# Kernel tuning notes

Measured on AMD Instinct MI355X. Metric: run time of the kernel, lower is better.

## Reference

```python
import jax, jax.numpy as jnp
import numpy as np

S, B, N, H = 64, 32, 325, 64

def setup_inputs() -> dict:
    key = jax.random.key(0)
    k1, k2, k3, k4 = jax.random.split(key, 4)
    return {
        "encoder_outputs": jax.random.normal(k1, (S, B, N, H), dtype=jnp.float32),
        "decoder_hidden": jax.random.normal(k2, (B, N, H), dtype=jnp.float32),
        "W": jax.random.normal(k3, (H, H), dtype=jnp.float32) * (1.0 / np.sqrt(H)),
        "b": jax.random.normal(k4, (H,), dtype=jnp.float32) * 0.01,
    }

def reference(encoder_outputs, decoder_hidden, W, b):
    # energy: (S,B,N,H) -- Linear + tanh
    energy = jnp.tanh(jnp.einsum('sbnh,kh->sbnk', encoder_outputs, W) + b)
    # broadcast multiply by decoder_hidden (B,N,H) and reduce over hidden dim -> (S,B,N)
    e = jnp.einsum('sbnh,bnh->sbn', energy, decoder_hidden)
    # softmax over seq_len, output (B,N,S)
    return jax.nn.softmax(jnp.transpose(e, (1, 2, 0)), axis=-1)
```

## Files before the change

### kernel.cpp

```cpp
#include <hip/hip_runtime.h>


constexpr int S = 64, B = 32, N = 325, H = 64;
constexpr int BN = B * N;
constexpr int SBN = S * BN;

typedef __attribute__((ext_vector_type(8))) short short8;
typedef __attribute__((ext_vector_type(4))) float f32x4;

union FragU { unsigned u[4]; short8 s8; uint4 v4; };

__device__ inline unsigned pack_hi(float x0, float x1, float& r0, float& r1) {
    unsigned u0 = __builtin_bit_cast(unsigned, x0);
    unsigned u1 = __builtin_bit_cast(unsigned, x1);
    r0 = x0 - __builtin_bit_cast(float, u0 & 0xffff0000u);
    r1 = x1 - __builtin_bit_cast(float, u1 & 0xffff0000u);
    return (u0 >> 16) | (u1 & 0xffff0000u);
}
__device__ inline unsigned pack_bf(float x0, float x1) {
    return (__builtin_bit_cast(unsigned, x0) >> 16) |
           (__builtin_bit_cast(unsigned, x1) & 0xffff0000u);
}

__global__ void pack_w(const float* __restrict__ W, uint4* __restrict__ wp) {
    int idx = blockIdx.x * blockDim.x + threadIdx.x;
    if (idx >= 512) return;
    int q = idx >> 7, kc = (idx >> 6) & 1, lane = idx & 63;
    int col = lane & 15, grp = lane >> 4;
    const float4* wpt = (const float4*)(W + (q * 16 + col) * H + kc * 32 + grp * 8);
    float4 w0 = wpt[0], w1 = wpt[1];
    float r0, r1, r2, r3, r4, r5, r6, r7;
    FragU hi, lo;
    hi.u[0] = pack_hi(w0.x, w0.y, r0, r1);
    hi.u[1] = pack_hi(w0.z, w0.w, r2, r3);
    hi.u[2] = pack_hi(w1.x, w1.y, r4, r5);
    hi.u[3] = pack_hi(w1.z, w1.w, r6, r7);
    lo.u[0] = pack_bf(r0, r1); lo.u[1] = pack_bf(r2, r3);
    lo.u[2] = pack_bf(r4, r5); lo.u[3] = pack_bf(r6, r7);
    wp[((q * 2 + kc) * 2 + 0) * 64 + lane] = hi.v4;
    wp[((q * 2 + kc) * 2 + 1) * 64 + lane] = lo.v4;
}

__global__ __launch_bounds__(256) void energy_k(
    const float* __restrict__ enc, const float* __restrict__ dec,
    const float* __restrict__ bias, const uint4* __restrict__ wp,
    float* __restrict__ e)
{
    const int lane = threadIdx.x & 63;
    const int wv   = threadIdx.x >> 6;
    const int col  = lane & 15, grp = lane >> 4;
    const int row0 = (blockIdx.x * 4 + wv) * 32;

    FragU a_hi[2][2], a_lo[2][2];
#pragma unroll
    for (int mt = 0; mt < 2; ++mt) {
        const float* er = enc + (row0 + mt * 16 + col) * H;
#pragma unroll
        for (int kc = 0; kc < 2; ++kc) {
            const float4* p4 = (const float4*)(er + kc * 32 + grp * 8);
            float4 x0 = p4[0], x1 = p4[1];
            float r0, r1, r2, r3, r4, r5, r6, r7;
            a_hi[mt][kc].u[0] = pack_hi(x0.x, x0.y, r0, r1);
            a_hi[mt][kc].u[1] = pack_hi(x0.z, x0.w, r2, r3);
            a_hi[mt][kc].u[2] = pack_hi(x1.x, x1.y, r4, r5);
            a_hi[mt][kc].u[3] = pack_hi(x1.z, x1.w, r6, r7);
            a_lo[mt][kc].u[0] = pack_bf(r0, r1);
            a_lo[mt][kc].u[1] = pack_bf(r2, r3);
            a_lo[mt][kc].u[2] = pack_bf(r4, r5);
            a_lo[mt][kc].u[3] = pack_bf(r6, r7);
        }
    }

    int doff[2][4];
#pragma unroll
    for (int mt = 0; mt < 2; ++mt)
#pragma unroll
        for (int r = 0; r < 4; ++r) {
            unsigned sbn = (unsigned)(row0 + mt * 16 + grp * 4 + r);
            unsigned bn  = sbn % (unsigned)BN;
            doff[mt][r]  = (int)(bn * H) + col;
        }

    float bias_v[4];
#pragma unroll
    for (int q = 0; q < 4; ++q) bias_v[q] = bias[q * 16 + col];

    float part[2][4];
#pragma unroll
    for (int mt = 0; mt < 2; ++mt)
#pragma unroll
        for (int r = 0; r < 4; ++r) part[mt][r] = 0.0f;

#pragma unroll
    for (int q = 0; q < 4; ++q) {
        f32x4 acc[2];
        acc[0] = (f32x4){0.f, 0.f, 0.f, 0.f};
        acc[1] = (f32x4){0.f, 0.f, 0.f, 0.f};
#pragma unroll
        for (int kc = 0; kc < 2; ++kc) {
            FragU bh, bl;
            bh.v4 = wp[((q * 2 + kc) * 2 + 0) * 64 + lane];
            bl.v4 = wp[((q * 2 + kc) * 2 + 1) * 64 + lane];
#pragma unroll
            for (int mt = 0; mt < 2; ++mt) {
                acc[mt] = __builtin_amdgcn_mfma_f32_16x16x32_bf16(a_hi[mt][kc].s8, bh.s8, acc[mt], 0, 0, 0);
                acc[mt] = __builtin_amdgcn_mfma_f32_16x16x32_bf16(a_lo[mt][kc].s8, bh.s8, acc[mt], 0, 0, 0);
                acc[mt] = __builtin_amdgcn_mfma_f32_16x16x32_bf16(a_hi[mt][kc].s8, bl.s8, acc[mt], 0, 0, 0);
            }
        }
#pragma unroll
        for (int mt = 0; mt < 2; ++mt)
#pragma unroll
            for (int r = 0; r < 4; ++r) {
                float a = acc[mt][r] + bias_v[q];
                float t = 1.0f - 2.0f * __builtin_amdgcn_rcpf(__expf(2.0f * a) + 1.0f);
                part[mt][r] = fmaf(t, dec[doff[mt][r] + q * 16], part[mt][r]);
            }
    }

#pragma unroll
    for (int mt = 0; mt < 2; ++mt)
#pragma unroll
        for (int r = 0; r < 4; ++r) {
            float v = part[mt][r];
            v += __shfl_xor(v, 1, 64);
            v += __shfl_xor(v, 2, 64);
            v += __shfl_xor(v, 4, 64);
            v += __shfl_xor(v, 8, 64);
            part[mt][r] = v;
        }

    float va = (col & 1) ? part[0][1] : part[0][0];
    float vb = (col & 1) ? part[0][3] : part[0][2];
    float vc = (col & 1) ? part[1][1] : part[1][0];
    float vd = (col & 1) ? part[1][3] : part[1][2];
    float ve = (col & 2) ? vb : va;
    float vf = (col & 2) ? vd : vc;
    float vo = (col & 4) ? vf : ve;
    if (col < 8)
        e[row0 + ((col >> 2) & 1) * 16 + grp * 4 + (col & 3)] = vo;
}

__global__ __launch_bounds__(256) void softmax_k(
    const float* __restrict__ e,
    float* __restrict__ out)
{
    __shared__ float Et[64 * 65];
    __shared__ float Mred[4][64], Sred[4][64], Mfin[64], Rfin[64];

    const int t = threadIdx.x;
    const int bn0 = blockIdx.x * 64;
    const int lane = t & 63, w = t >> 6;

#pragma unroll
    for (int i = 0; i < 16; ++i) {
        int s = w * 16 + i;
        float v = (bn0 + lane < BN) ? e[s * BN + bn0 + lane] : 0.0f;
        Et[s * 65 + lane] = v;
    }
    __syncthreads();

    {
        const int bn_loc = t & 63, sq = t >> 6;
        float m = -1e30f;
#pragma unroll
        for (int i = 0; i < 16; ++i)
            m = fmaxf(m, Et[(sq * 16 + i) * 65 + bn_loc]);
        Mred[sq][bn_loc] = m;
    }
    __syncthreads();
    {
        const int bn_loc = t & 63, sq = t >> 6;
        float m = fmaxf(fmaxf(Mred[0][bn_loc], Mred[1][bn_loc]),
                        fmaxf(Mred[2][bn_loc], Mred[3][bn_loc]));
        float sum = 0.0f;
#pragma unroll
        for (int i = 0; i < 16; ++i)
            sum += __expf(Et[(sq * 16 + i) * 65 + bn_loc] - m);
        Sred[sq][bn_loc] = sum;
        if (sq == 0) Mfin[bn_loc] = m;
    }
    __syncthreads();
    if ((t >> 6) == 0) {
        const int bn_loc = t & 63;
        float sum = Sred[0][bn_loc] + Sred[1][bn_loc] + Sred[2][bn_loc] + Sred[3][bn_loc];
        Rfin[bn_loc] = __builtin_amdgcn_rcpf(sum);
    }
    __syncthreads();

    const int s_out = t & 63, bq = t >> 6;
#pragma unroll
    for (int j = 0; j < 16; ++j) {
        int bn_loc = bq * 16 + j;
        if (bn0 + bn_loc < BN) {
            float p = __expf(Et[s_out * 65 + bn_loc] - Mfin[bn_loc]) * Rfin[bn_loc];
            out[(bn0 + bn_loc) * S + s_out] = p;
        }
    }
}

extern "C" void kernel_launch(void* const* d_in, const int* in_sizes, int n_in,
                              void* d_out, int out_size, void* d_ws, size_t ws_size,
                              hipStream_t stream) {
    const float* enc  = (const float*)d_in[0];
    const float* dec  = (const float*)d_in[1];
    const float* W    = (const float*)d_in[2];
    const float* bias = (const float*)d_in[3];
    float* out        = (float*)d_out;

    uint4* wp = (uint4*)d_ws;
    float* e  = (float*)((char*)d_ws + 65536);

    pack_w<<<2, 256, 0, stream>>>(W, wp);
    energy_k<<<SBN / 128, 256, 0, stream>>>(enc, dec, bias, wp, e);
    softmax_k<<<(BN + 63) / 64, 256, 0, stream>>>(e, out);
}
```

Before: 254.0 us.

## Process four row tiles per wave with register prefetch of next encoder tile

```diff
diff --git a/kernel.cpp b/kernel.cpp
--- a/kernel.cpp
+++ b/kernel.cpp
@@ -4,6 +4,8 @@
 constexpr int S = 64, B = 32, N = 325, H = 64;
 constexpr int BN = B * N;
 constexpr int SBN = S * BN;
+constexpr int NWAVE = SBN / 128;
+constexpr int NBLK = NWAVE / 4;
 
 typedef __attribute__((ext_vector_type(8))) short short8;
 typedef __attribute__((ext_vector_type(4))) float f32x4;
@@ -49,96 +51,136 @@
     const int lane = threadIdx.x & 63;
     const int wv   = threadIdx.x >> 6;
     const int col  = lane & 15, grp = lane >> 4;
-    const int row0 = (blockIdx.x * 4 + wv) * 32;
-
-    FragU a_hi[2][2], a_lo[2][2];
-#pragma unroll
-    for (int mt = 0; mt < 2; ++mt) {
-        const float* er = enc + (row0 + mt * 16 + col) * H;
-#pragma unroll
-        for (int kc = 0; kc < 2; ++kc) {
-            const float4* p4 = (const float4*)(er + kc * 32 + grp * 8);
-            float4 x0 = p4[0], x1 = p4[1];
-            float r0, r1, r2, r3, r4, r5, r6, r7;
-            a_hi[mt][kc].u[0] = pack_hi(x0.x, x0.y, r0, r1);
-            a_hi[mt][kc].u[1] = pack_hi(x0.z, x0.w, r2, r3);
-            a_hi[mt][kc].u[2] = pack_hi(x1.x, x1.y, r4, r5);
-            a_hi[mt][kc].u[3] = pack_hi(x1.z, x1.w, r6, r7);
-            a_lo[mt][kc].u[0] = pack_bf(r0, r1);
-            a_lo[mt][kc].u[1] = pack_bf(r2, r3);
-            a_lo[mt][kc].u[2] = pack_bf(r4, r5);
-            a_lo[mt][kc].u[3] = pack_bf(r6, r7);
-        }
-    }
-
-    int doff[2][4];
-#pragma unroll
-    for (int mt = 0; mt < 2; ++mt)
-#pragma unroll
-        for (int r = 0; r < 4; ++r) {
-            unsigned sbn = (unsigned)(row0 + mt * 16 + grp * 4 + r);
-            unsigned bn  = sbn % (unsigned)BN;
-            doff[mt][r]  = (int)(bn * H) + col;
-        }
+    const int wave_id = blockIdx.x * 4 + wv;
+    const int row_base = wave_id * 128;
 
     float bias_v[4];
 #pragma unroll
     for (int q = 0; q < 4; ++q) bias_v[q] = bias[q * 16 + col];
 
-    float part[2][4];
-#pragma unroll
-    for (int mt = 0; mt < 2; ++mt)
-#pragma unroll
-        for (int r = 0; r < 4; ++r) part[mt][r] = 0.0f;
-
-#pragma unroll
-    for (int q = 0; q < 4; ++q) {
-        f32x4 acc[2];
-        acc[0] = (f32x4){0.f, 0.f, 0.f, 0.f};
-        acc[1] = (f32x4){0.f, 0.f, 0.f, 0.f};
-#pragma unroll
-        for (int kc = 0; kc < 2; ++kc) {
-            FragU bh, bl;
-            bh.v4 = wp[((q * 2 + kc) * 2 + 0) * 64 + lane];
-            bl.v4 = wp[((q * 2 + kc) * 2 + 1) * 64 + lane];
+    float4 raw[8];
+
+    {
+#pragma unroll
+        for (int mt = 0; mt < 2; ++mt) {
+            const float4* er = (const float4*)(enc + (size_t)(row_base + mt * 16 + col) * H) + grp * 2;
+#pragma unroll
+            for (int kc = 0; kc < 2; ++kc) {
+                raw[mt * 4 + kc * 2 + 0] = er[kc * 8 + 0];
+                raw[mt * 4 + kc * 2 + 1] = er[kc * 8 + 1];
+            }
+        }
+    }
+
+    unsigned bnv[2][4];
+
+#pragma unroll
+    for (int t = 0; t < 4; ++t) {
+        const int row0 = row_base + t * 32;
+
+        FragU a_hi[2][2], a_lo[2][2];
+#pragma unroll
+        for (int mt = 0; mt < 2; ++mt)
+#pragma unroll
+            for (int kc = 0; kc < 2; ++kc) {
+                float4 x0 = raw[mt * 4 + kc * 2 + 0];
+                float4 x1 = raw[mt * 4 + kc * 2 + 1];
+                float r0, r1, r2, r3, r4, r5, r6, r7;
+                a_hi[mt][kc].u[0] = pack_hi(x0.x, x0.y, r0, r1);
+                a_hi[mt][kc].u[1] = pack_hi(x0.z, x0.w, r2, r3);
+                a_hi[mt][kc].u[2] = pack_hi(x1.x, x1.y, r4, r5);
+                a_hi[mt][kc].u[3] = pack_hi(x1.z, x1.w, r6, r7);
+                a_lo[mt][kc].u[0] = pack_bf(r0, r1);
+                a_lo[mt][kc].u[1] = pack_bf(r2, r3);
+                a_lo[mt][kc].u[2] = pack_bf(r4, r5);
+                a_lo[mt][kc].u[3] = pack_bf(r6, r7);
+            }
+
+        if (t < 3) {
+            const int rown = row_base + (t + 1) * 32;
 #pragma unroll
             for (int mt = 0; mt < 2; ++mt) {
-                acc[mt] = __builtin_amdgcn_mfma_f32_16x16x32_bf16(a_hi[mt][kc].s8, bh.s8, acc[mt], 0, 0, 0);
-                acc[mt] = __builtin_amdgcn_mfma_f32_16x16x32_bf16(a_lo[mt][kc].s8, bh.s8, acc[mt], 0, 0, 0);
-                acc[mt] = __builtin_amdgcn_mfma_f32_16x16x32_bf16(a_hi[mt][kc].s8, bl.s8, acc[mt], 0, 0, 0);
-            }
-        }
+                const float4* er = (const float4*)(enc + (size_t)(rown + mt * 16 + col) * H) + grp * 2;
+#pragma unroll
+                for (int kc = 0; kc < 2; ++kc) {
+                    raw[mt * 4 + kc * 2 + 0] = er[kc * 8 + 0];
+                    raw[mt * 4 + kc * 2 + 1] = er[kc * 8 + 1];
+                }
+            }
+        }
+
+        int doff[2][4];
 #pragma unroll
         for (int mt = 0; mt < 2; ++mt)
 #pragma unroll
             for (int r = 0; r < 4; ++r) {
-                float a = acc[mt][r] + bias_v[q];
-                float t = 1.0f - 2.0f * __builtin_amdgcn_rcpf(__expf(2.0f * a) + 1.0f);
-                part[mt][r] = fmaf(t, dec[doff[mt][r] + q * 16], part[mt][r]);
-            }
-    }
-
-#pragma unroll
-    for (int mt = 0; mt < 2; ++mt)
-#pragma unroll
-        for (int r = 0; r < 4; ++r) {
-            float v = part[mt][r];
-            v += __shfl_xor(v, 1, 64);
-            v += __shfl_xor(v, 2, 64);
-            v += __shfl_xor(v, 4, 64);
-            v += __shfl_xor(v, 8, 64);
-            part[mt][r] = v;
-        }
-
-    float va = (col & 1) ? part[0][1] : part[0][0];
-    float vb = (col & 1) ? part[0][3] : part[0][2];
-    float vc = (col & 1) ? part[1][1] : part[1][0];
-    float vd = (col & 1) ? part[1][3] : part[1][2];
-    float ve = (col & 2) ? vb : va;
-    float vf = (col & 2) ? vd : vc;
-    float vo = (col & 4) ? vf : ve;
-    if (col < 8)
-        e[row0 + ((col >> 2) & 1) * 16 + grp * 4 + (col & 3)] = vo;
+                if (t == 0) {
+                    unsigned sbn = (unsigned)(row0 + mt * 16 + grp * 4 + r);
+                    bnv[mt][r] = sbn % (unsigned)BN;
+                } else {
+                    unsigned b2 = bnv[mt][r] + 32u;
+                    bnv[mt][r] = (b2 >= (unsigned)BN) ? b2 - (unsigned)BN : b2;
+                }
+                doff[mt][r] = (int)(bnv[mt][r] * (unsigned)H) + col;
+            }
+
+        float part[2][4];
+#pragma unroll
+        for (int mt = 0; mt < 2; ++mt)
+#pragma unroll
+            for (int r = 0; r < 4; ++r) part[mt][r] = 0.0f;
+
+#pragma unroll
+        for (int q = 0; q < 4; ++q) {
+            f32x4 acc[2];
+            acc[0] = (f32x4){0.f, 0.f, 0.f, 0.f};
+            acc[1] = (f32x4){0.f, 0.f, 0.f, 0.f};
+#pragma unroll
+            for (int kc = 0; kc < 2; ++kc) {
+                FragU bh, bl;
+                bh.v4 = wp[((q * 2 + kc) * 2 + 0) * 64 + lane];
+                bl.v4 = wp[((q * 2 + kc) * 2 + 1) * 64 + lane];
+#pragma unroll
+                for (int mt = 0; mt < 2; ++mt) {
+                    acc[mt] = __builtin_amdgcn_mfma_f32_16x16x32_bf16(a_hi[mt][kc].s8, bh.s8, acc[mt], 0, 0, 0);
+                    acc[mt] = __builtin_amdgcn_mfma_f32_16x16x32_bf16(a_lo[mt][kc].s8, bh.s8, acc[mt], 0, 0, 0);
+                    acc[mt] = __builtin_amdgcn_mfma_f32_16x16x32_bf16(a_hi[mt][kc].s8, bl.s8, acc[mt], 0, 0, 0);
+                }
+            }
+#pragma unroll
+            for (int mt = 0; mt < 2; ++mt)
+#pragma unroll
+                for (int r = 0; r < 4; ++r) {
+                    float a = acc[mt][r] + bias_v[q];
+                    float z = __builtin_amdgcn_exp2f(a * 2.8853900817779268f);
+                    float rr = __builtin_amdgcn_rcpf(z + 1.0f);
+                    float tt = fmaf(-2.0f, rr, 1.0f);
+                    part[mt][r] = fmaf(tt, dec[doff[mt][r] + q * 16], part[mt][r]);
+                }
+        }
+
+#pragma unroll
+        for (int mt = 0; mt < 2; ++mt)
+#pragma unroll
+            for (int r = 0; r < 4; ++r) {
+                float v = part[mt][r];
+                v += __shfl_xor(v, 1, 64);
+                v += __shfl_xor(v, 2, 64);
+                v += __shfl_xor(v, 4, 64);
+                v += __shfl_xor(v, 8, 64);
+                part[mt][r] = v;
+            }
+
+        float va = (col & 1) ? part[0][1] : part[0][0];
+        float vb = (col & 1) ? part[0][3] : part[0][2];
+        float vc = (col & 1) ? part[1][1] : part[1][0];
+        float vd = (col & 1) ? part[1][3] : part[1][2];
+        float ve = (col & 2) ? vb : va;
+        float vf = (col & 2) ? vd : vc;
+        float vo = (col & 4) ? vf : ve;
+        if (col < 8)
+            e[row0 + ((col >> 2) & 1) * 16 + grp * 4 + (col & 3)] = vo;
+    }
 }
 
 __global__ __launch_bounds__(256) void softmax_k(
@@ -212,6 +254,6 @@
     float* e  = (float*)((char*)d_ws + 65536);
 
     pack_w<<<2, 256, 0, stream>>>(W, wp);
-    energy_k<<<SBN / 128, 256, 0, stream>>>(enc, dec, bias, wp, e);
+    energy_k<<<NBLK, 256, 0, stream>>>(enc, dec, bias, wp, e);
     softmax_k<<<(BN + 63) / 64, 256, 0, stream>>>(e, out);
 }
```

After: 294.4 us. 15.9% more time.
